# Performance work log

Measured on AMD Instinct MI355X. Metric: run time of the kernel, lower is better.

Reference implementation:

```python
import jax, jax.numpy as jnp
import numpy as np

N = 10000      # nodes
E = 160000     # edges (before self-loops)
F_IN = 128     # num_features
H1, D1 = 4, 256   # conv1: 4 heads x 256, concat -> 1024
D2 = 256          # conv2: 1 head x 256
NEG_SLOPE = 0.2


def setup_inputs() -> dict:
    key = jax.random.key(0)
    ks = jax.random.split(key, 12)
    def p(k, shape, fan):
        return jax.random.normal(k, shape, jnp.float32) / np.float32(np.sqrt(fan))
    return {
        "x": jax.random.normal(ks[0], (N, F_IN), jnp.float32),
        "edge_index": jax.random.randint(ks[1], (2, E), 0, N, jnp.int32),
        "W1": p(ks[2], (F_IN, H1 * D1), F_IN),
        "att_src1": p(ks[3], (H1, D1), D1),
        "att_dst1": p(ks[4], (H1, D1), D1),
        "b1": jnp.zeros((H1 * D1,), jnp.float32),
        "lin1_W": p(ks[5], (F_IN, H1 * D1), F_IN),
        "lin1_b": jnp.zeros((H1 * D1,), jnp.float32),
        "W2": p(ks[6], (H1 * D1, D2), H1 * D1),
        "att_src2": p(ks[7], (1, D2), D2),
        "att_dst2": p(ks[8], (1, D2), D2),
        "b2": jnp.zeros((D2,), jnp.float32),
        "lin2_W": p(ks[9], (H1 * D1, D2), H1 * D1),
        "lin2_b": jnp.zeros((D2,), jnp.float32),
    }


def gat_layer(x, src, dst, W, a_src, a_dst, b, heads, d):
    """PyG-style GATConv: transform, edgewise LeakyReLU attention,
    segment-softmax over destination neighborhoods, scatter-add, concat heads."""
    n = x.shape[0]
    h = (x @ W).reshape(n, heads, d)                       # [N, H, D]
    s_src = jnp.einsum('nhd,hd->nh', h, a_src)             # per-node scores
    s_dst = jnp.einsum('nhd,hd->nh', h, a_dst)
    e = jax.nn.leaky_relu(s_src[src] + s_dst[dst], NEG_SLOPE)   # [E, H]
    m = jax.ops.segment_max(e, dst, num_segments=n)        # stable softmax per dst
    p = jnp.exp(e - m[dst])
    z = jax.ops.segment_sum(p, dst, num_segments=n)
    alpha = p / (z[dst] + 1e-16)                           # [E, H]
    msg = h[src] * alpha[:, :, None]                       # [E, H, D]
    out = jax.ops.segment_sum(msg, dst, num_segments=n)    # [N, H, D]
    return out.reshape(n, heads * d) + b, alpha


def reference(x, edge_index, W1, att_src1, att_dst1, b1, lin1_W, lin1_b,
              W2, att_src2, att_dst2, b2, lin2_W, lin2_b):
    n = x.shape[0]
    loop = jnp.arange(n, dtype=edge_index.dtype)           # add self-loops (PyG default)
    src = jnp.concatenate([edge_index[0], loop])
    dst = jnp.concatenate([edge_index[1], loop])
    h1, alpha1 = gat_layer(x, src, dst, W1, att_src1, att_dst1, b1, H1, D1)
    h1 = jax.nn.elu(h1 + x @ lin1_W + lin1_b)              # conv1 + lin1 residual, ELU
    h2, _ = gat_layer(h1, src, dst, W2, att_src2, att_dst2, b2, 1, D2)
    out = h2 + h1 @ lin2_W + lin2_b                        # conv2 + lin2 residual
    return out, alpha1
```

## Files before the change

kernel.cpp:

```cpp
#include <hip/hip_runtime.h>
#include <hip/hip_bf16.h>
#include <math.h>

#define NN   10000
#define EE   160000
#define ETOT 170000
#define FIN  128
#define C1   1024
#define NH1  4
#define D1   256
#define D2   256
#define MAXD 96

typedef __attribute__((ext_vector_type(8))) short bf16x8;
typedef __attribute__((ext_vector_type(4))) float f32x4;

__device__ __forceinline__ float b2f(unsigned short u)
{
    union { unsigned int i; float f; } c; c.i = (unsigned int)u << 16; return c.f;
}
__device__ __forceinline__ unsigned short f2b(float x)
{
    return __builtin_bit_cast(unsigned short, __float2bfloat16(x));
}
__device__ __forceinline__ void split1(float x, unsigned short &h, unsigned short &l)
{
    __hip_bfloat16 hb = __float2bfloat16(x);
    float r = x - __bfloat162float(hb);
    h = __builtin_bit_cast(unsigned short, hb);
    l = __builtin_bit_cast(unsigned short, __float2bfloat16(r));
}

__device__ __forceinline__ void split_A_body(const float* __restrict__ X,
                                             unsigned short* __restrict__ A2,
                                             int M, int K, int idx)
{
    int kq4 = K >> 2;
    if (idx >= M * kq4) return;
    int m = idx / kq4, kq = idx % kq4;
    float4 v = *(const float4*)&X[(size_t)m * K + kq * 4];
    ushort4 h, l;
    split1(v.x, h.x, l.x); split1(v.y, h.y, l.y);
    split1(v.z, h.z, l.z); split1(v.w, h.w, l.w);
    unsigned short* row = A2 + (size_t)m * (2 * K);
    *(ushort4*)&row[kq * 4]     = h;
    *(ushort4*)&row[K + kq * 4] = l;
}

__device__ __forceinline__ void split_Bt_body(const float* __restrict__ B0,
                                              const float* __restrict__ B1,
                                              int K, int N0, int Ntot,
                                              unsigned short* __restrict__ Bt, int idx)
{
    int total = Ntot * (K >> 2);
    if (idx >= total) return;
    int n = idx % Ntot;
    int kq = idx / Ntot;
    int k = kq * 4;
    const float* B; int nc, nb;
    if (n < N0) { B = B0; nc = n; nb = N0; }
    else        { B = B1; nc = n - N0; nb = Ntot - N0; }
    float v0 = B[(size_t)(k + 0) * nb + nc];
    float v1 = B[(size_t)(k + 1) * nb + nc];
    float v2 = B[(size_t)(k + 2) * nb + nc];
    float v3 = B[(size_t)(k + 3) * nb + nc];
    ushort4 h, l;
    split1(v0, h.x, l.x); split1(v1, h.y, l.y);
    split1(v2, h.z, l.z); split1(v3, h.w, l.w);
    unsigned short* row = Bt + (size_t)n * (3 * K);
    *(ushort4*)&row[k]         = h;
    *(ushort4*)&row[K + k]     = h;
    *(ushort4*)&row[2 * K + k] = l;
}

__global__ __launch_bounds__(256)
void prep(const float* __restrict__ x, unsigned short* __restrict__ A1stk,
          const float* __restrict__ W1, const float* __restrict__ lin1_W,
          unsigned short* __restrict__ Bt1,
          const float* __restrict__ W2, const float* __restrict__ lin2_W,
          unsigned short* __restrict__ Bt2,
          const int* __restrict__ dstp, int* __restrict__ cnt)
{
    const int b = blockIdx.x, t = threadIdx.x;
    if (b < 1250) {
        split_A_body(x, A1stk, NN, FIN, b * 256 + t);
    } else if (b < 1506) {
        split_Bt_body(W1, lin1_W, FIN, C1, 2048, Bt1, (b - 1250) * 256 + t);
    } else if (b < 2018) {
        split_Bt_body(W2, lin2_W, C1, D2, 512, Bt2, (b - 1506) * 256 + t);
    } else {
        int e = (b - 2018) * 256 + t;
        if (e < ETOT) {
            int d = (e < EE) ? dstp[e] : (e - EE);
            atomicAdd(&cnt[d], 1);
        }
    }
}

__device__ __forceinline__ void glds16(const void* g, void* l)
{
    __builtin_amdgcn_global_load_lds((const __attribute__((address_space(1))) void*)g,
                                     (__attribute__((address_space(3))) void*)l, 16, 0, 0);
}

template<int BN, int WM, int WN, int BK>
__global__ __launch_bounds__(256)
void gemm_split(const unsigned short* __restrict__ A, int lda, int ka2,
                const unsigned short* __restrict__ Bt, int keff,
                unsigned short* __restrict__ outPb, float* __restrict__ outR,
                int M, int nsplit, int ldR, int ntn,
                const float* __restrict__ bias0, const float* __restrict__ bias1)
{
    constexpr int BM   = 128;
    constexpr int WTM  = BM / WM,  WTN = BN / WN;
    constexpr int FJ   = WTM / 16, FI  = WTN / 16;
    constexpr int KS   = BK / 32;
    constexpr int SLOTS = BK / 8;
    constexpr int SMASK = SLOTS - 1;
    constexpr int SWSH  = (BK == 32) ? 1 : 0;
    constexpr int RPC  = 512 / BK;
    constexpr int ACH  = BM / RPC;
    constexpr int NCH  = (BM + BN) / RPC;
    constexpr int CPW  = NCH / 4;
    constexpr int ABUF = BM * BK, BBUF = BN * BK;

    __shared__ __align__(16) unsigned short sA[2 * ABUF];
    __shared__ __align__(16) unsigned short sB[2 * BBUF];

    const int tid = threadIdx.x;
    const int w = tid >> 6, lane = tid & 63;

    const int cpx = gridDim.x >> 3;
    const int t0  = (blockIdx.x & 7) * cpx + (blockIdx.x >> 3);
    const int m0 = (t0 / ntn) * BM;
    const int n0 = (t0 % ntn) * BN;
    const int wm = w / WN, wn = w % WN;

    f32x4 acc[FI][FJ] = {};

    const unsigned short* gp[CPW];
    int lofs[CPW];
    bool isa[CPW];
    {
        const int r  = lane / SLOTS;
        const int sl = lane % SLOTS;
        const int ssl = sl ^ ((r >> SWSH) & SMASK);
        #pragma unroll
        for (int cc = 0; cc < CPW; ++cc) {
            int c = w * CPW + cc;
            if (c < ACH) {
                int gm = m0 + c * RPC + r; if (gm >= M) gm = M - 1;
                gp[cc]   = A + (size_t)gm * lda + ssl * 8;
                lofs[cc] = c * 512;
                isa[cc]  = true;
            } else {
                int gn = n0 + (c - ACH) * RPC + r;
                gp[cc]   = Bt + (size_t)gn * keff + ssl * 8;
                lofs[cc] = (c - ACH) * 512;
                isa[cc]  = false;
            }
        }
    }

    const int rAl = wm * WTM + (lane & 15);
    const int rBl = wn * WTN + (lane & 15);
    const int koff = (lane >> 4) * 8;
    const int nit = keff / BK;
    int cur = 0;

    #pragma unroll
    for (int cc = 0; cc < CPW; ++cc)
        glds16(gp[cc], (isa[cc] ? sA : sB) + lofs[cc]);
    __syncthreads();

    for (int it = 0; it < nit; ++it) {
        if (it + 1 < nit) {
            int kn = (it + 1) * BK;
            int kAn = (kn >= ka2) ? (kn - ka2) : kn;
            #pragma unroll
            for (int cc = 0; cc < CPW; ++cc) {
                unsigned short* dst = (isa[cc] ? sA + (cur ^ 1) * ABUF
                                               : sB + (cur ^ 1) * BBUF) + lofs[cc];
                glds16(gp[cc] + (isa[cc] ? kAn : kn), dst);
            }
        }
        const unsigned short* cA = sA + cur * ABUF;
        const unsigned short* cB = sB + cur * BBUF;
        #pragma unroll
        for (int ks = 0; ks < KS; ++ks) {
            const int sIdx = (ks * 32 + koff) >> 3;
            bf16x8 av[FJ], bv[FI];
            #pragma unroll
            for (int f = 0; f < FI; ++f) {
                int row = rBl + f * 16;
                bv[f] = *(const bf16x8*)&cB[row * BK + ((sIdx ^ ((row >> SWSH) & SMASK)) << 3)];
            }
            #pragma unroll
            for (int f = 0; f < FJ; ++f) {
                int row = rAl + f * 16;
                av[f] = *(const bf16x8*)&cA[row * BK + ((sIdx ^ ((row >> SWSH) & SMASK)) << 3)];
            }
            #pragma unroll
            for (int fj = 0; fj < FJ; ++fj)
                #pragma unroll
                for (int fi = 0; fi < FI; ++fi)
                    acc[fi][fj] = __builtin_amdgcn_mfma_f32_16x16x32_bf16(
                        bv[fi], av[fj], acc[fi][fj], 0, 0, 0);
        }
        __syncthreads();
        cur ^= 1;
    }

    const int lrow = lane & 15;
    const int lcol = (lane >> 4) << 2;
    #pragma unroll
    for (int fj = 0; fj < FJ; ++fj) {
        int row = m0 + wm * WTM + fj * 16 + lrow;
        if (row >= M) continue;
        #pragma unroll
        for (int fi = 0; fi < FI; ++fi) {
            int col = n0 + wn * WTN + fi * 16 + lcol;
            f32x4 v = acc[fi][fj];
            if (col < nsplit) {
                ushort4 o;
                o.x = f2b(v[0]); o.y = f2b(v[1]); o.z = f2b(v[2]); o.w = f2b(v[3]);
                *(ushort4*)&outPb[(size_t)row * nsplit + col] = o;
            } else {
                int c = col - nsplit;
                const float4 g0 = *(const float4*)&bias0[c];
                const float4 g1 = *(const float4*)&bias1[c];
                v[0] += g0.x + g1.x; v[1] += g0.y + g1.y;
                v[2] += g0.z + g1.z; v[3] += g0.w + g1.w;
                *(f32x4*)&outR[(size_t)row * ldR + c] = v;
            }
        }
    }
}

__global__ __launch_bounds__(256)
void scores_h4(const unsigned short* __restrict__ h, const float* __restrict__ a_src,
               const float* __restrict__ a_dst, float* __restrict__ s_src,
               float* __restrict__ s_dst)
{
    const int n = blockIdx.x;
    const int w = threadIdx.x >> 6;
    const int lane = threadIdx.x & 63;
    ushort4 u = *(const ushort4*)&h[(size_t)n * C1 + w * D1 + lane * 4];
    float4 as = ((const float4*)&a_src[w * D1])[lane];
    float4 ad = ((const float4*)&a_dst[w * D1])[lane];
    float vx = b2f(u.x), vy = b2f(u.y), vz = b2f(u.z), vw = b2f(u.w);
    float ss = vx * as.x + vy * as.y + vz * as.z + vw * as.w;
    float sd = vx * ad.x + vy * ad.y + vz * ad.z + vw * ad.w;
    #pragma unroll
    for (int off = 32; off; off >>= 1) {
        ss += __shfl_xor(ss, off);
        sd += __shfl_xor(sd, off);
    }
    if (lane == 0) { s_src[n * NH1 + w] = ss; s_dst[n * NH1 + w] = sd; }
}

__global__ __launch_bounds__(256)
void scores_h1(const unsigned short* __restrict__ h, const float* __restrict__ a_src,
               const float* __restrict__ a_dst, float* __restrict__ s_src,
               float* __restrict__ s_dst)
{
    const int n = blockIdx.x * 4 + (threadIdx.x >> 6);
    if (n >= NN) return;
    const int lane = threadIdx.x & 63;
    ushort4 u = *(const ushort4*)&h[(size_t)n * D2 + lane * 4];
    float4 as = ((const float4*)a_src)[lane];
    float4 ad = ((const float4*)a_dst)[lane];
    float vx = b2f(u.x), vy = b2f(u.y), vz = b2f(u.z), vw = b2f(u.w);
    float ss = vx * as.x + vy * as.y + vz * as.z + vw * as.w;
    float sd = vx * ad.x + vy * ad.y + vz * ad.z + vw * ad.w;
    #pragma unroll
    for (int off = 32; off; off >>= 1) {
        ss += __shfl_xor(ss, off);
        sd += __shfl_xor(sd, off);
    }
    if (lane == 0) { s_src[n] = ss; s_dst[n] = sd; }
}

__global__ __launch_bounds__(1024)
void scan_kernel(const int* __restrict__ cnt, int* __restrict__ row_ptr)
{
    __shared__ int part[1024];
    const int t = threadIdx.x;
    int local[10];
    int s = 0;
    #pragma unroll
    for (int j = 0; j < 10; ++j) {
        int idx = t * 10 + j;
        local[j] = s;
        s += (idx < NN) ? cnt[idx] : 0;
    }
    part[t] = s;
    __syncthreads();
    for (int off = 1; off < 1024; off <<= 1) {
        int v = (t >= off) ? part[t - off] : 0;
        __syncthreads();
        part[t] += v;
        __syncthreads();
    }
    int prefix = (t > 0) ? part[t - 1] : 0;
    #pragma unroll
    for (int j = 0; j < 10; ++j) {
        int idx = t * 10 + j;
        if (idx < NN) row_ptr[idx] = prefix + local[j];
    }
    if (t == 0) row_ptr[NN] = ETOT;
}

__global__ void scatter_edges(const int* __restrict__ srcp, const int* __restrict__ dstp,
                              const int* __restrict__ row_ptr, int* __restrict__ fill,
                              int* __restrict__ csr_src, int* __restrict__ csr_eid)
{
    int e = blockIdx.x * 256 + threadIdx.x;
    if (e >= ETOT) return;
    int s, d;
    if (e < EE) { s = srcp[e]; d = dstp[e]; } else { s = d = e - EE; }
    int pos = row_ptr[d] + atomicAdd(&fill[d], 1);
    csr_src[pos] = s;
    csr_eid[pos] = e;
}

__global__ __launch_bounds__(256)
void sort_segments(const int* __restrict__ row_ptr, int* __restrict__ csr_src,
                   int* __restrict__ csr_eid)
{
    const int n = blockIdx.x * 4 + (threadIdx.x >> 6);
    if (n >= NN) return;
    const int lane = threadIdx.x & 63;
    const int start = row_ptr[n], end = row_ptr[n + 1];
    const int deg = end - start;
    if (deg > 64) return;
    unsigned int key = 0xFFFFFFFFu;
    if (lane < deg)
        key = ((unsigned)csr_src[start + lane] << 18) | (unsigned)csr_eid[start + lane];
    #pragma unroll
    for (int k = 2; k <= 64; k <<= 1) {
        #pragma unroll
        for (int j = k >> 1; j > 0; j >>= 1) {
            unsigned int pk = (unsigned int)__shfl_xor((int)key, j);
            bool wantMin = (((lane & k) == 0) == ((lane & j) == 0));
            key = wantMin ? (key < pk ? key : pk) : (key > pk ? key : pk);
        }
    }
    if (lane < deg) {
        csr_src[start + lane] = (int)(key >> 18);
        csr_eid[start + lane] = (int)(key & 0x3FFFFu);
    }
}

__global__ __launch_bounds__(256)
void aggregate1(const unsigned short* __restrict__ h1b, const float* __restrict__ s_src,
                const float* __restrict__ s_dst,
                const int* __restrict__ row_ptr, const int* __restrict__ csr_src,
                const int* __restrict__ csr_eid, const float* __restrict__ base_in,
                unsigned short* __restrict__ a2stk, float* __restrict__ alpha_out)
{
    __shared__ float lalpha[NH1][MAXD];
    const int n = blockIdx.x;
    const int t = threadIdx.x;
    const int h = t >> 6;
    const int lane = t & 63;
    const int start = row_ptr[n], end = row_ptr[n + 1];
    const float sd = s_dst[n * NH1 + h];

    float m = -1e30f;
    for (int i = start + lane; i < end; i += 64) {
        float sc = s_src[csr_src[i] * NH1 + h] + sd;
        sc = sc > 0.f ? sc : 0.2f * sc;
        m = fmaxf(m, sc);
    }
    #pragma unroll
    for (int off = 32; off; off >>= 1) m = fmaxf(m, __shfl_xor(m, off));
    float z = 0.f;
    for (int i = start + lane; i < end; i += 64) {
        float sc = s_src[csr_src[i] * NH1 + h] + sd;
        sc = sc > 0.f ? sc : 0.2f * sc;
        z += __expf(sc - m);
    }
    #pragma unroll
    for (int off = 32; off; off >>= 1) z += __shfl_xor(z, off);
    const float invz = 1.f / (z + 1e-16f);
    for (int i = start + lane; i < end; i += 64) {
        float sc = s_src[csr_src[i] * NH1 + h] + sd;
        sc = sc > 0.f ? sc : 0.2f * sc;
        float a = __expf(sc - m) * invz;
        alpha_out[(size_t)csr_eid[i] * NH1 + h] = a;
        int idx = i - start;
        if (idx < MAXD) lalpha[h][idx] = a;
    }
    __syncthreads();

    float4 base = *(const float4*)&base_in[(size_t)n * C1 + t * 4];
    float4 acc = make_float4(0.f, 0.f, 0.f, 0.f);
    for (int i = start; i < end; ++i) {
        const int s = csr_src[i];
        const int idx = i - start;
        float a;
        if (idx < MAXD) {
            a = lalpha[h][idx];
        } else {
            float sc = s_src[s * NH1 + h] + sd;
            sc = sc > 0.f ? sc : 0.2f * sc;
            a = __expf(sc - m) * invz;
        }
        ushort4 v = *(const ushort4*)&h1b[(size_t)s * C1 + t * 4];
        acc.x += a * b2f(v.x); acc.y += a * b2f(v.y);
        acc.z += a * b2f(v.z); acc.w += a * b2f(v.w);
    }
    float4 r;
    r.x = acc.x + base.x; r.y = acc.y + base.y;
    r.z = acc.z + base.z; r.w = acc.w + base.w;
    r.x = r.x > 0.f ? r.x : expm1f(r.x);
    r.y = r.y > 0.f ? r.y : expm1f(r.y);
    r.z = r.z > 0.f ? r.z : expm1f(r.z);
    r.w = r.w > 0.f ? r.w : expm1f(r.w);
    __syncthreads();
    ushort4 hi, lo;
    split1(r.x, hi.x, lo.x); split1(r.y, hi.y, lo.y);
    split1(r.z, hi.z, lo.z); split1(r.w, hi.w, lo.w);
    unsigned short* row = a2stk + (size_t)n * (2 * C1);
    *(ushort4*)&row[t * 4]      = hi;
    *(ushort4*)&row[C1 + t * 4] = lo;
}

__global__ __launch_bounds__(64)
void aggregate2(const unsigned short* __restrict__ h2b, const float* __restrict__ s_src,
                const float* __restrict__ s_dst,
                const int* __restrict__ row_ptr, const int* __restrict__ csr_src,
                const float* __restrict__ accin, float* __restrict__ out)
{
    __shared__ float lalpha[MAXD];
    const int n = blockIdx.x;
    const int t = threadIdx.x;
    const int start = row_ptr[n], end = row_ptr[n + 1];
    const float sd = s_dst[n];

    float m = -1e30f;
    for (int i = start + t; i < end; i += 64) {
        float sc = s_src[csr_src[i]] + sd;
        sc = sc > 0.f ? sc : 0.2f * sc;
        m = fmaxf(m, sc);
    }
    #pragma unroll
    for (int off = 32; off; off >>= 1) m = fmaxf(m, __shfl_xor(m, off));
    float z = 0.f;
    for (int i = start + t; i < end; i += 64) {
        float sc = s_src[csr_src[i]] + sd;
        sc = sc > 0.f ? sc : 0.2f * sc;
        z += __expf(sc - m);
    }
    #pragma unroll
    for (int off = 32; off; off >>= 1) z += __shfl_xor(z, off);
    const float invz = 1.f / (z + 1e-16f);
    for (int i = start + t; i < end; i += 64) {
        float sc = s_src[csr_src[i]] + sd;
        sc = sc > 0.f ? sc : 0.2f * sc;
        int idx = i - start;
        if (idx < MAXD) lalpha[idx] = __expf(sc - m) * invz;
    }
    __syncthreads();

    float4 acc = make_float4(0.f, 0.f, 0.f, 0.f);
    for (int i = start; i < end; ++i) {
        const int s = csr_src[i];
        const int idx = i - start;
        float a;
        if (idx < MAXD) {
            a = lalpha[idx];
        } else {
            float sc = s_src[s] + sd;
            sc = sc > 0.f ? sc : 0.2f * sc;
            a = __expf(sc - m) * invz;
        }
        ushort4 v = *(const ushort4*)&h2b[(size_t)s * D2 + t * 4];
        acc.x += a * b2f(v.x); acc.y += a * b2f(v.y);
        acc.z += a * b2f(v.z); acc.w += a * b2f(v.w);
    }
    float4 base = *(const float4*)&accin[(size_t)n * D2 + t * 4];
    float4 r;
    r.x = acc.x + base.x; r.y = acc.y + base.y;
    r.z = acc.z + base.z; r.w = acc.w + base.w;
    *(float4*)&out[(size_t)n * D2 + t * 4] = r;
}

extern "C" void kernel_launch(void* const* d_in, const int* in_sizes, int n_in,
                              void* d_out, int out_size, void* d_ws, size_t ws_size,
                              hipStream_t stream)
{
    const float* x        = (const float*)d_in[0];
    const int*   ei       = (const int*)  d_in[1];
    const float* W1       = (const float*)d_in[2];
    const float* att_src1 = (const float*)d_in[3];
    const float* att_dst1 = (const float*)d_in[4];
    const float* b1       = (const float*)d_in[5];
    const float* lin1_W   = (const float*)d_in[6];
    const float* lin1_b   = (const float*)d_in[7];
    const float* W2       = (const float*)d_in[8];
    const float* att_src2 = (const float*)d_in[9];
    const float* att_dst2 = (const float*)d_in[10];
    const float* b2       = (const float*)d_in[11];
    const float* lin2_W   = (const float*)d_in[12];
    const float* lin2_b   = (const float*)d_in[13];
    const int* srcp = ei;
    const int* dstp = ei + EE;

    float* out    = (float*)d_out;
    float* alpha1 = out + (size_t)NN * D2;

    float* fw = (float*)d_ws;
    float* acc1   = fw;   fw += (size_t)NN * C1;
    unsigned short* h1b = (unsigned short*)fw; fw += (size_t)NN * C1 / 2;
    unsigned short* h2b = (unsigned short*)fw; fw += (size_t)NN * D2 / 2;
    float* acc2   = fw;   fw += (size_t)NN * D2;
    unsigned short* A1stk = (unsigned short*)fw; fw += (size_t)NN * FIN;
    unsigned short* Bt1   = (unsigned short*)fw; fw += (size_t)2048 * 3 * FIN / 2;
    unsigned short* Bt2   = (unsigned short*)fw; fw += (size_t)512 * 3 * C1 / 2;
    float* s_src1 = fw;   fw += NN * NH1;
    float* s_dst1 = fw;   fw += NN * NH1;
    float* s_src2 = fw;   fw += NN;
    float* s_dst2 = fw;   fw += NN;
    int* ip      = (int*)fw;
    int* cnt     = ip;    ip += NN;
    int* fill    = ip;    ip += NN;
    int* row_ptr = ip;    ip += NN + 4;
    int* csr_src = ip;    ip += ETOT;
    int* csr_eid = ip;    ip += ETOT;

    unsigned short* A2stk = (unsigned short*)acc1;

    hipMemsetAsync(cnt, 0, 2 * NN * sizeof(int), stream);

    const int mt = (NN + 127) / 128;

    prep<<<2683, 256, 0, stream>>>(x, A1stk, W1, lin1_W, Bt1, W2, lin2_W, Bt2, dstp, cnt);

    scan_kernel<<<1, 1024, 0, stream>>>(cnt, row_ptr);
    scatter_edges<<<(ETOT + 255) / 256, 256, 0, stream>>>(srcp, dstp, row_ptr, fill,
                                                          csr_src, csr_eid);
    sort_segments<<<(NN + 3) / 4, 256, 0, stream>>>(row_ptr, csr_src, csr_eid);

    gemm_split<128, 2, 2, 32><<<mt * 16, 256, 0, stream>>>(
        A1stk, 2 * FIN, 2 * FIN, Bt1, 3 * FIN, h1b, acc1, NN, C1, C1, 16, lin1_b, b1);
    scores_h4<<<NN, 256, 0, stream>>>(h1b, att_src1, att_dst1, s_src1, s_dst1);

    aggregate1<<<NN, 256, 0, stream>>>(h1b, s_src1, s_dst1, row_ptr, csr_src, csr_eid,
                                       acc1, A2stk, alpha1);

    gemm_split<64, 4, 1, 64><<<mt * 8, 256, 0, stream>>>(
        A2stk, 2 * C1, 2 * C1, Bt2, 3 * C1, h2b, acc2, NN, D2, D2, 8, lin2_b, b2);

    scores_h1<<<(NN + 3) / 4, 256, 0, stream>>>(h2b, att_src2, att_dst2, s_src2, s_dst2);
    aggregate2<<<NN, 64, 0, stream>>>(h2b, s_src2, s_dst2, row_ptr, csr_src, acc2, out);
}
```

Measured before the change: 236.9 us.

## Aggregate layer-1 in input space before projection, fold attention vectors into weights

Uses linearity to reorder layer 1: attention scores come from x times precomputed W1·att vectors, neighbor aggregation is done on the 128-wide input features per head, and a single fused GEMM then multiplies the aggregated inputs and x by W1 and lin1_W with bias and ELU in the epilogue. This removes the gather of 1024-wide h1 rows per edge and the separate fp32 accumulator round trip. Layer-2 scores are likewise computed from h1 through W2·att vectors, and the segment sort kernel is dropped. The risks are a changed floating-point summation order, since the sort that fixed edge order is gone, and a GEMM with a larger K per output tile.

```diff
diff --git a/kernel.cpp b/kernel.cpp
--- a/kernel.cpp
+++ b/kernel.cpp
@@ -73,27 +73,74 @@
     *(ushort4*)&row[2 * K + k] = l;
 }
 
+__device__ __forceinline__ void split_Bt1_body(const float* __restrict__ W1,
+                                               const float* __restrict__ lin1W,
+                                               unsigned short* __restrict__ Bt, int idx)
+{
+    if (idx >= 1024 * 64) return;
+    int n = idx & 1023;
+    int k = (idx >> 10) * 4;
+    float v[4];
+    #pragma unroll
+    for (int i = 0; i < 4; ++i) {
+        int kk = k + i;
+        v[i] = (kk < 128) ? W1[(size_t)kk * C1 + n] : lin1W[(size_t)(kk - 128) * C1 + n];
+    }
+    ushort4 h, l;
+    split1(v[0], h.x, l.x); split1(v[1], h.y, l.y);
+    split1(v[2], h.z, l.z); split1(v[3], h.w, l.w);
+    unsigned short* row = Bt + (size_t)n * 768;
+    *(ushort4*)&row[k]       = h;
+    *(ushort4*)&row[256 + k] = h;
+    *(ushort4*)&row[512 + k] = l;
+}
+
 __global__ __launch_bounds__(256)
 void prep(const float* __restrict__ x, unsigned short* __restrict__ A1stk,
           const float* __restrict__ W1, const float* __restrict__ lin1_W,
           unsigned short* __restrict__ Bt1,
           const float* __restrict__ W2, const float* __restrict__ lin2_W,
           unsigned short* __restrict__ Bt2,
-          const int* __restrict__ dstp, int* __restrict__ cnt)
+          const int* __restrict__ dstp, int* __restrict__ cnt,
+          const float* __restrict__ as1, const float* __restrict__ ad1,
+          float* __restrict__ w1s, float* __restrict__ w1d,
+          const float* __restrict__ as2, const float* __restrict__ ad2,
+          float* __restrict__ v2s, float* __restrict__ v2d)
 {
     const int b = blockIdx.x, t = threadIdx.x;
+    const int w = t >> 6, lane = t & 63;
     if (b < 1250) {
         split_A_body(x, A1stk, NN, FIN, b * 256 + t);
     } else if (b < 1506) {
-        split_Bt_body(W1, lin1_W, FIN, C1, 2048, Bt1, (b - 1250) * 256 + t);
+        split_Bt1_body(W1, lin1_W, Bt1, (b - 1250) * 256 + t);
     } else if (b < 2018) {
         split_Bt_body(W2, lin2_W, C1, D2, 512, Bt2, (b - 1506) * 256 + t);
-    } else {
+    } else if (b < 2683) {
         int e = (b - 2018) * 256 + t;
         if (e < ETOT) {
             int d = (e < EE) ? dstp[e] : (e - EE);
             atomicAdd(&cnt[d], 1);
         }
+    } else if (b < 2939) {
+        int gw = (b - 2683) * 4 + w;
+        int k = gw >> 3, rem = gw & 7, h = rem >> 1, issd = rem & 1;
+        const float* a = issd ? ad1 : as1;
+        float4 wv = *(const float4*)&W1[(size_t)k * C1 + h * 256 + lane * 4];
+        float4 av = *(const float4*)&a[h * 256 + lane * 4];
+        float s = wv.x * av.x + wv.y * av.y + wv.z * av.z + wv.w * av.w;
+        #pragma unroll
+        for (int off = 32; off; off >>= 1) s += __shfl_xor(s, off);
+        if (lane == 0) (issd ? w1d : w1s)[k * 4 + h] = s;
+    } else {
+        int gw = (b - 2939) * 4 + w;
+        int k = gw >> 1, issd = gw & 1;
+        const float* a = issd ? ad2 : as2;
+        float4 wv = *(const float4*)&W2[(size_t)k * D2 + lane * 4];
+        float4 av = *(const float4*)&a[lane * 4];
+        float s = wv.x * av.x + wv.y * av.y + wv.z * av.z + wv.w * av.w;
+        #pragma unroll
+        for (int off = 32; off; off >>= 1) s += __shfl_xor(s, off);
+        if (lane == 0) (issd ? v2d : v2s)[k] = s;
     }
 }
 
@@ -101,6 +148,125 @@
 {
     __builtin_amdgcn_global_load_lds((const __attribute__((address_space(1))) void*)g,
                                      (__attribute__((address_space(3))) void*)l, 16, 0, 0);
+}
+
+__global__ __launch_bounds__(256)
+void gemm_l1(const unsigned short* __restrict__ Apx,
+             const unsigned short* __restrict__ Ax,
+             const unsigned short* __restrict__ Bt,
+             unsigned short* __restrict__ h1split,
+             int M, const float* __restrict__ bias0, const float* __restrict__ bias1)
+{
+    constexpr int BM = 128, BN = 128, BK = 32;
+    constexpr int FJ = 4, FI = 4;
+    constexpr int SLOTS = 4, SMASK = 3, SWSH = 1;
+    constexpr int RPC = 16, ACH = 8, CPW = 4;
+    constexpr int ABUF = BM * BK, BBUF = BN * BK;
+    __shared__ __align__(16) unsigned short sA[2 * ABUF];
+    __shared__ __align__(16) unsigned short sB[2 * BBUF];
+    const int tid = threadIdx.x, w = tid >> 6, lane = tid & 63;
+    const int cpx = gridDim.x >> 3;
+    const int t0 = (blockIdx.x & 7) * cpx + (blockIdx.x >> 3);
+    const int m0 = (t0 >> 3) * BM;
+    const int n0 = (t0 & 7) * BN;
+    const int hsel = n0 >> 8;
+    const int wm = w >> 1, wn = w & 1;
+    f32x4 acc[FI][FJ] = {};
+
+    const unsigned short *gx[CPW], *gpx[CPW], *gb[CPW];
+    int lofs[CPW]; bool isa[CPW];
+    {
+        const int r = lane / SLOTS, sl = lane % SLOTS;
+        const int ssl = sl ^ ((r >> SWSH) & SMASK);
+        #pragma unroll
+        for (int cc = 0; cc < CPW; ++cc) {
+            int c = w * CPW + cc;
+            if (c < ACH) {
+                int gm = m0 + c * RPC + r; if (gm >= M) gm = M - 1;
+                gx[cc]  = Ax  + (size_t)gm * 256 + ssl * 8;
+                gpx[cc] = Apx + (size_t)gm * 1024 + hsel * 256 + ssl * 8;
+                gb[cc]  = nullptr;
+                lofs[cc] = c * 512;
+                isa[cc] = true;
+            } else {
+                int gn = n0 + (c - ACH) * RPC + r;
+                gx[cc] = gpx[cc] = nullptr;
+                gb[cc] = Bt + (size_t)gn * 768 + ssl * 8;
+                lofs[cc] = (c - ACH) * 512;
+                isa[cc] = false;
+            }
+        }
+    }
+
+    const int rAl = wm * 64 + (lane & 15);
+    const int rBl = wn * 64 + (lane & 15);
+    const int sIdx = lane >> 4;
+    const int nit = 768 / BK;
+    int cur = 0;
+
+    auto stage = [&](int kk, int buf) {
+        int rr = kk >> 7;
+        bool px = !(rr & 1);
+        int off = px ? ((rr == 2) ? 128 : 0) : ((rr == 3) ? 128 : 0);
+        int kin = kk & 127;
+        #pragma unroll
+        for (int cc = 0; cc < CPW; ++cc) {
+            if (isa[cc]) glds16((px ? gpx[cc] : gx[cc]) + off + kin, sA + buf * ABUF + lofs[cc]);
+            else         glds16(gb[cc] + kk,                         sB + buf * BBUF + lofs[cc]);
+        }
+    };
+
+    stage(0, 0);
+    __syncthreads();
+    for (int it = 0; it < nit; ++it) {
+        if (it + 1 < nit) stage((it + 1) * BK, cur ^ 1);
+        const unsigned short* cA = sA + cur * ABUF;
+        const unsigned short* cB = sB + cur * BBUF;
+        bf16x8 av[FJ], bv[FI];
+        #pragma unroll
+        for (int f = 0; f < FI; ++f) {
+            int row = rBl + f * 16;
+            bv[f] = *(const bf16x8*)&cB[row * BK + ((sIdx ^ ((row >> SWSH) & SMASK)) << 3)];
+        }
+        #pragma unroll
+        for (int f = 0; f < FJ; ++f) {
+            int row = rAl + f * 16;
+            av[f] = *(const bf16x8*)&cA[row * BK + ((sIdx ^ ((row >> SWSH) & SMASK)) << 3)];
+        }
+        #pragma unroll
+        for (int fj = 0; fj < FJ; ++fj)
+            #pragma unroll
+            for (int fi = 0; fi < FI; ++fi)
+                acc[fi][fj] = __builtin_amdgcn_mfma_f32_16x16x32_bf16(
+                    bv[fi], av[fj], acc[fi][fj], 0, 0, 0);
+        __syncthreads();
+        cur ^= 1;
+    }
+
+    const int lrow = lane & 15;
+    const int lcol = (lane >> 4) << 2;
+    #pragma unroll
+    for (int fj = 0; fj < FJ; ++fj) {
+        int row = m0 + wm * 64 + fj * 16 + lrow;
+        if (row >= M) continue;
+        #pragma unroll
+        for (int fi = 0; fi < FI; ++fi) {
+            int col = n0 + wn * 64 + fi * 16 + lcol;
+            f32x4 v = acc[fi][fj];
+            const float4 g0 = *(const float4*)&bias0[col];
+            const float4 g1 = *(const float4*)&bias1[col];
+            v[0] += g0.x + g1.x; v[1] += g0.y + g1.y;
+            v[2] += g0.z + g1.z; v[3] += g0.w + g1.w;
+            #pragma unroll
+            for (int i = 0; i < 4; ++i) v[i] = v[i] > 0.f ? v[i] : expm1f(v[i]);
+            ushort4 hi, lo;
+            split1(v[0], hi.x, lo.x); split1(v[1], hi.y, lo.y);
+            split1(v[2], hi.z, lo.z); split1(v[3], hi.w, lo.w);
+            unsigned short* orow = h1split + (size_t)row * 2048;
+            *(ushort4*)&orow[col]        = hi;
+            *(ushort4*)&orow[C1 + col]   = lo;
+        }
+    }
 }
 
 template<int BN, int WM, int WN, int BK>
@@ -238,41 +404,55 @@
 }
 
 __global__ __launch_bounds__(256)
-void scores_h4(const unsigned short* __restrict__ h, const float* __restrict__ a_src,
-               const float* __restrict__ a_dst, float* __restrict__ s_src,
-               float* __restrict__ s_dst)
-{
-    const int n = blockIdx.x;
-    const int w = threadIdx.x >> 6;
-    const int lane = threadIdx.x & 63;
-    ushort4 u = *(const ushort4*)&h[(size_t)n * C1 + w * D1 + lane * 4];
-    float4 as = ((const float4*)&a_src[w * D1])[lane];
-    float4 ad = ((const float4*)&a_dst[w * D1])[lane];
-    float vx = b2f(u.x), vy = b2f(u.y), vz = b2f(u.z), vw = b2f(u.w);
-    float ss = vx * as.x + vy * as.y + vz * as.z + vw * as.w;
-    float sd = vx * ad.x + vy * ad.y + vz * ad.z + vw * ad.w;
-    #pragma unroll
-    for (int off = 32; off; off >>= 1) {
-        ss += __shfl_xor(ss, off);
-        sd += __shfl_xor(sd, off);
-    }
-    if (lane == 0) { s_src[n * NH1 + w] = ss; s_dst[n * NH1 + w] = sd; }
-}
-
-__global__ __launch_bounds__(256)
-void scores_h1(const unsigned short* __restrict__ h, const float* __restrict__ a_src,
-               const float* __restrict__ a_dst, float* __restrict__ s_src,
+void s1_scores(const float* __restrict__ x, const float* __restrict__ w1s,
+               const float* __restrict__ w1d, float* __restrict__ s_src,
                float* __restrict__ s_dst)
 {
     const int n = blockIdx.x * 4 + (threadIdx.x >> 6);
     if (n >= NN) return;
     const int lane = threadIdx.x & 63;
-    ushort4 u = *(const ushort4*)&h[(size_t)n * D2 + lane * 4];
-    float4 as = ((const float4*)a_src)[lane];
-    float4 ad = ((const float4*)a_dst)[lane];
-    float vx = b2f(u.x), vy = b2f(u.y), vz = b2f(u.z), vw = b2f(u.w);
-    float ss = vx * as.x + vy * as.y + vz * as.z + vw * as.w;
-    float sd = vx * ad.x + vy * ad.y + vz * ad.z + vw * ad.w;
+    float2 xv = *(const float2*)&x[(size_t)n * FIN + lane * 2];
+    float4 wa = *(const float4*)&w1s[(lane * 2) * 4];
+    float4 wb = *(const float4*)&w1s[(lane * 2 + 1) * 4];
+    float4 da = *(const float4*)&w1d[(lane * 2) * 4];
+    float4 db = *(const float4*)&w1d[(lane * 2 + 1) * 4];
+    float ss[4] = { xv.x * wa.x + xv.y * wb.x, xv.x * wa.y + xv.y * wb.y,
+                    xv.x * wa.z + xv.y * wb.z, xv.x * wa.w + xv.y * wb.w };
+    float sd[4] = { xv.x * da.x + xv.y * db.x, xv.x * da.y + xv.y * db.y,
+                    xv.x * da.z + xv.y * db.z, xv.x * da.w + xv.y * db.w };
+    #pragma unroll
+    for (int off = 32; off; off >>= 1) {
+        #pragma unroll
+        for (int h = 0; h < 4; ++h) {
+            ss[h] += __shfl_xor(ss[h], off);
+            sd[h] += __shfl_xor(sd[h], off);
+        }
+    }
+    if (lane == 0) {
+        #pragma unroll
+        for (int h = 0; h < 4; ++h) {
+            s_src[n * NH1 + h] = ss[h];
+            s_dst[n * NH1 + h] = sd[h];
+        }
+    }
+}
+
+__global__ __launch_bounds__(256)
+void scores2(const unsigned short* __restrict__ h1split, const float* __restrict__ v2s,
+             const float* __restrict__ v2d, float* __restrict__ s_src,
+             float* __restrict__ s_dst)
+{
+    const int n = blockIdx.x * 4 + (threadIdx.x >> 6);
+    if (n >= NN) return;
+    const int lane = threadIdx.x & 63;
+    const unsigned short* row = h1split + (size_t)n * 2048 + lane * 16;
+    float ss = 0.f, sd = 0.f;
+    #pragma unroll
+    for (int q = 0; q < 16; ++q) {
+        float hv = b2f(row[q]);
+        ss += hv * v2s[lane * 16 + q];
+        sd += hv * v2d[lane * 16 + q];
+    }
     #pragma unroll
     for (int off = 32; off; off >>= 1) {
         ss += __shfl_xor(ss, off);
@@ -325,39 +505,10 @@
 }
 
 __global__ __launch_bounds__(256)
-void sort_segments(const int* __restrict__ row_ptr, int* __restrict__ csr_src,
-                   int* __restrict__ csr_eid)
-{
-    const int n = blockIdx.x * 4 + (threadIdx.x >> 6);
-    if (n >= NN) return;
-    const int lane = threadIdx.x & 63;
-    const int start = row_ptr[n], end = row_ptr[n + 1];
-    const int deg = end - start;
-    if (deg > 64) return;
-    unsigned int key = 0xFFFFFFFFu;
-    if (lane < deg)
-        key = ((unsigned)csr_src[start + lane] << 18) | (unsigned)csr_eid[start + lane];
-    #pragma unroll
-    for (int k = 2; k <= 64; k <<= 1) {
-        #pragma unroll
-        for (int j = k >> 1; j > 0; j >>= 1) {
-            unsigned int pk = (unsigned int)__shfl_xor((int)key, j);
-            bool wantMin = (((lane & k) == 0) == ((lane & j) == 0));
-            key = wantMin ? (key < pk ? key : pk) : (key > pk ? key : pk);
-        }
-    }
-    if (lane < deg) {
-        csr_src[start + lane] = (int)(key >> 18);
-        csr_eid[start + lane] = (int)(key & 0x3FFFFu);
-    }
-}
-
-__global__ __launch_bounds__(256)
-void aggregate1(const unsigned short* __restrict__ h1b, const float* __restrict__ s_src,
-                const float* __restrict__ s_dst,
-                const int* __restrict__ row_ptr, const int* __restrict__ csr_src,
-                const int* __restrict__ csr_eid, const float* __restrict__ base_in,
-                unsigned short* __restrict__ a2stk, float* __restrict__ alpha_out)
+void px_gather(const unsigned short* __restrict__ Ax, const float* __restrict__ s_src,
+               const float* __restrict__ s_dst, const int* __restrict__ row_ptr,
+               const int* __restrict__ csr_src, const int* __restrict__ csr_eid,
+               unsigned short* __restrict__ Apx, float* __restrict__ alpha_out)
 {
     __shared__ float lalpha[NH1][MAXD];
     const int n = blockIdx.x;
@@ -394,8 +545,7 @@
     }
     __syncthreads();
 
-    float4 base = *(const float4*)&base_in[(size_t)n * C1 + t * 4];
-    float4 acc = make_float4(0.f, 0.f, 0.f, 0.f);
+    float p0 = 0.f, p1 = 0.f;
     for (int i = start; i < end; ++i) {
         const int s = csr_src[i];
         const int idx = i - start;
@@ -407,24 +557,18 @@
             sc = sc > 0.f ? sc : 0.2f * sc;
             a = __expf(sc - m) * invz;
         }
-        ushort4 v = *(const ushort4*)&h1b[(size_t)s * C1 + t * 4];
-        acc.x += a * b2f(v.x); acc.y += a * b2f(v.y);
-        acc.z += a * b2f(v.z); acc.w += a * b2f(v.w);
-    }
-    float4 r;
-    r.x = acc.x + base.x; r.y = acc.y + base.y;
-    r.z = acc.z + base.z; r.w = acc.w + base.w;
-    r.x = r.x > 0.f ? r.x : expm1f(r.x);
-    r.y = r.y > 0.f ? r.y : expm1f(r.y);
-    r.z = r.z > 0.f ? r.z : expm1f(r.z);
-    r.w = r.w > 0.f ? r.w : expm1f(r.w);
-    __syncthreads();
-    ushort4 hi, lo;
-    split1(r.x, hi.x, lo.x); split1(r.y, hi.y, lo.y);
-    split1(r.z, hi.z, lo.z); split1(r.w, hi.w, lo.w);
-    unsigned short* row = a2stk + (size_t)n * (2 * C1);
-    *(ushort4*)&row[t * 4]      = hi;
-    *(ushort4*)&row[C1 + t * 4] = lo;
+        const unsigned short* xr = Ax + (size_t)s * 256 + lane * 2;
+        ushort2 xh = *(const ushort2*)xr;
+        ushort2 xl = *(const ushort2*)(xr + 128);
+        p0 += a * (b2f(xh.x) + b2f(xl.x));
+        p1 += a * (b2f(xh.y) + b2f(xl.y));
+    }
+    ushort2 hi, lo;
+    split1(p0, hi.x, lo.x);
+    split1(p1, hi.y, lo.y);
+    unsigned short* orow = Apx + (size_t)n * 1024 + h * 256 + lane * 2;
+    *(ushort2*)orow         = hi;
+    *(ushort2*)(orow + 128) = lo;
 }
 
 __global__ __launch_bounds__(64)
@@ -512,47 +656,48 @@
     float* alpha1 = out + (size_t)NN * D2;
 
     float* fw = (float*)d_ws;
-    float* acc1   = fw;   fw += (size_t)NN * C1;
-    unsigned short* h1b = (unsigned short*)fw; fw += (size_t)NN * C1 / 2;
-    unsigned short* h2b = (unsigned short*)fw; fw += (size_t)NN * D2 / 2;
-    float* acc2   = fw;   fw += (size_t)NN * D2;
-    unsigned short* A1stk = (unsigned short*)fw; fw += (size_t)NN * FIN;
-    unsigned short* Bt1   = (unsigned short*)fw; fw += (size_t)2048 * 3 * FIN / 2;
-    unsigned short* Bt2   = (unsigned short*)fw; fw += (size_t)512 * 3 * C1 / 2;
-    float* s_src1 = fw;   fw += NN * NH1;
-    float* s_dst1 = fw;   fw += NN * NH1;
-    float* s_src2 = fw;   fw += NN;
-    float* s_dst2 = fw;   fw += NN;
+    unsigned short* A1stk = (unsigned short*)fw; fw += (size_t)NN * 256 / 2;
+    unsigned short* Apx   = (unsigned short*)fw; fw += (size_t)NN * 1024 / 2;
+    unsigned short* A2stk = (unsigned short*)fw; fw += (size_t)NN * 2048 / 2;
+    unsigned short* h2b   = (unsigned short*)fw; fw += (size_t)NN * 256 / 2;
+    float* acc2   = fw;  fw += (size_t)NN * D2;
+    unsigned short* Bt1 = (unsigned short*)fw; fw += (size_t)1024 * 768 / 2;
+    unsigned short* Bt2 = (unsigned short*)fw; fw += (size_t)512 * 3072 / 2;
+    float* w1s = fw; fw += 512;
+    float* w1d = fw; fw += 512;
+    float* v2s = fw; fw += 1024;
+    float* v2d = fw; fw += 1024;
+    float* s_src1 = fw; fw += NN * NH1;
+    float* s_dst1 = fw; fw += NN * NH1;
+    float* s_src2 = fw; fw += NN;
+    float* s_dst2 = fw; fw += NN;
     int* ip      = (int*)fw;
-    int* cnt     = ip;    ip += NN;
-    int* fill    = ip;    ip += NN;
-    int* row_ptr = ip;    ip += NN + 4;
-    int* csr_src = ip;    ip += ETOT;
-    int* csr_eid = ip;    ip += ETOT;
-
-    unsigned short* A2stk = (unsigned short*)acc1;
+    int* cnt     = ip;  ip += NN;
+    int* fill    = ip;  ip += NN;
+    int* row_ptr = ip;  ip += NN + 4;
+    int* csr_src = ip;  ip += ETOT;
+    int* csr_eid = ip;  ip += ETOT;
 
     hipMemsetAsync(cnt, 0, 2 * NN * sizeof(int), stream);
 
-    const int mt = (NN + 127) / 128;
-
-    prep<<<2683, 256, 0, stream>>>(x, A1stk, W1, lin1_W, Bt1, W2, lin2_W, Bt2, dstp, cnt);
+    prep<<<3451, 256, 0, stream>>>(x, A1stk, W1, lin1_W, Bt1, W2, lin2_W, Bt2,
+                                   dstp, cnt, att_src1, att_dst1, w1s, w1d,
+                                   att_src2, att_dst2, v2s, v2d);
 
     scan_kernel<<<1, 1024, 0, stream>>>(cnt, row_ptr);
     scatter_edges<<<(ETOT + 255) / 256, 256, 0, stream>>>(srcp, dstp, row_ptr, fill,
                                                           csr_src, csr_eid);
-    sort_segments<<<(NN + 3) / 4, 256, 0, stream>>>(row_ptr, csr_src, csr_eid);
-
-    gemm_split<128, 2, 2, 32><<<mt * 16, 256, 0, stream>>>(
-        A1stk, 2 * FIN, 2 * FIN, Bt1, 3 * FIN, h1b, acc1, NN, C1, C1, 16, lin1_b, b1);
-    scores_h4<<<NN, 256, 0, stream>>>(h1b, att_src1, att_dst1, s_src1, s_dst1);
-
-    aggregate1<<<NN, 256, 0, stream>>>(h1b, s_src1, s_dst1, row_ptr, csr_src, csr_eid,
-                                       acc1, A2stk, alpha1);
-
-    gemm_split<64, 4, 1, 64><<<mt * 8, 256, 0, stream>>>(
+
+    s1_scores<<<(NN + 3) / 4, 256, 0, stream>>>(x, w1s, w1d, s_src1, s_dst1);
+    px_gather<<<NN, 256, 0, stream>>>(A1stk, s_src1, s_dst1, row_ptr, csr_src, csr_eid,
+                                      Apx, alpha1);
+
+    gemm_l1<<<79 * 8, 256, 0, stream>>>(Apx, A1stk, Bt1, A2stk, NN, lin1_b, b1);
+
+    scores2<<<(NN + 3) / 4, 256, 0, stream>>>(A2stk, v2s, v2d, s_src2, s_dst2);
+
+    gemm_split<64, 4, 1, 64><<<79 * 8, 256, 0, stream>>>(
         A2stk, 2 * C1, 2 * C1, Bt2, 3 * C1, h2b, acc2, NN, D2, D2, 8, lin2_b, b2);
 
-    scores_h1<<<(NN + 3) / 4, 256, 0, stream>>>(h2b, att_src2, att_dst2, s_src2, s_dst2);
     aggregate2<<<NN, 64, 0, stream>>>(h2b, s_src2, s_dst2, row_ptr, csr_src, acc2, out);
 }
```

After: 223.0 us. 1.06x faster.
